# Performance work log

Measured on AMD Instinct MI355X. Metric: run time of the kernel, lower is better.

Reference implementation:

```python
import jax, jax.numpy as jnp
import numpy as np

N_HEAD = 16

def setup_inputs() -> dict:
    key = jax.random.key(0)
    ks = jax.random.split(key, 5)
    B, T, C = 4, 2048, 1024
    s = 0.02
    return {
        "x": jax.random.normal(ks[0], (B, T, C), dtype=jnp.float32),
        "W_attn": jax.random.normal(ks[1], (C, 3 * C), dtype=jnp.float32) * s,
        "b_attn": jax.random.normal(ks[2], (3 * C,), dtype=jnp.float32) * s,
        "W_proj": jax.random.normal(ks[3], (C, C), dtype=jnp.float32) * s,
        "b_proj": jax.random.normal(ks[4], (C,), dtype=jnp.float32) * s,
    }

def reference(x, W_attn, b_attn, W_proj, b_proj):
    B, T, C = x.shape
    H = N_HEAD
    D = C // H
    qkv = x @ W_attn + b_attn                      # [B,T,3C]
    q, k, v = jnp.split(qkv, 3, axis=2)
    # [B,H,T,D]
    q = q.reshape(B, T, H, D).transpose(0, 2, 1, 3)
    k = k.reshape(B, T, H, D).transpose(0, 2, 1, 3)
    v = v.reshape(B, T, H, D).transpose(0, 2, 1, 3)
    scale = 1.0 / jnp.sqrt(jnp.float32(D))
    att = jnp.einsum('bhqd,bhkd->bhqk', q, k) * scale
    causal = jnp.tril(jnp.ones((T, T), dtype=bool))
    att = jnp.where(causal[None, None], att, -jnp.inf)
    att = jax.nn.softmax(att, axis=-1)
    y = jnp.einsum('bhqk,bhkd->bhqd', att, v)       # [B,H,T,D]
    y = y.transpose(0, 2, 1, 3).reshape(B, T, C)
    return y @ W_proj + b_proj
```

## Files before the change

### kernel.cpp

```cpp
#include <hip/hip_runtime.h>

typedef unsigned short u16;
typedef unsigned int u32;
typedef __bf16 bf16x8 __attribute__((ext_vector_type(8)));
typedef float f32x4 __attribute__((ext_vector_type(4)));

#define MFMA16(a,b,c) __builtin_amdgcn_mfma_f32_16x16x32_bf16((a),(b),(c),0,0,0)

__device__ __forceinline__ float b2f(u16 u) {
    u32 v = ((u32)u) << 16;
    return __builtin_bit_cast(float, v);
}
__device__ __forceinline__ u16 f2b(float f) {
    u32 u = __builtin_bit_cast(u32, f);
    u = u + 0x7FFFu + ((u >> 16) & 1u);
    return (u16)(u >> 16);
}

__device__ __forceinline__ void gload_lds16(const u16* g, u16* l) {
    __builtin_amdgcn_global_load_lds(
        (__attribute__((address_space(1))) void*)g,
        (__attribute__((address_space(3))) void*)l, 16, 0, 0);
}

__device__ __forceinline__ uint4 load8_bf16(const void* base, size_t off, int f32m) {
    if (f32m) {
        const float* p = (const float*)base + off;
        float4 a = *(const float4*)p;
        float4 b = *(const float4*)(p + 4);
        union { u16 u[8]; uint4 v; } t;
        t.u[0] = f2b(a.x); t.u[1] = f2b(a.y); t.u[2] = f2b(a.z); t.u[3] = f2b(a.w);
        t.u[4] = f2b(b.x); t.u[5] = f2b(b.y); t.u[6] = f2b(b.z); t.u[7] = f2b(b.w);
        return t.v;
    }
    return *(const uint4*)((const u16*)base + off);
}

__global__ __launch_bounds__(256) void k_detect(const u16* __restrict__ x, int* flag) {
    __shared__ int c;
    if (threadIdx.x == 0) c = 0;
    __syncthreads();
    int my = 0;
    #pragma unroll
    for (int j = 0; j < 16; ++j) {
        u16 v = x[2 * (threadIdx.x + 256 * j)];
        if (((v >> 7) & 0xFF) >= 0x90) ++my;
    }
    atomicAdd(&c, my);
    __syncthreads();
    if (threadIdx.x == 0) *flag = (c > 64) ? 1 : 0;
}

__global__ __launch_bounds__(256) void k_cvt_bias(
    const void* __restrict__ ba, const void* __restrict__ bp,
    const int* __restrict__ flag, u16* __restrict__ bac, u16* __restrict__ bpc)
{
    const int f32m = *flag;
    const int t = threadIdx.x;
    #pragma unroll
    for (int j = 0; j < 12; ++j) {
        int i = t + 256 * j;
        if (i < 3072) bac[i] = f32m ? f2b(((const float*)ba)[i]) : ((const u16*)ba)[i];
    }
    #pragma unroll
    for (int j = 0; j < 4; ++j) {
        int i = t + 256 * j;
        if (i < 1024) bpc[i] = f32m ? f2b(((const float*)bp)[i]) : ((const u16*)bp)[i];
    }
}

__global__ __launch_bounds__(256) void k_cvt_x(
    const float* __restrict__ x, const int* __restrict__ flag, u16* __restrict__ out)
{
    if (!*flag) return;
    size_t i = ((size_t)blockIdx.x * 256 + threadIdx.x) * 8;
    float4 a = *(const float4*)(x + i);
    float4 b = *(const float4*)(x + i + 4);
    union { u16 u[8]; uint4 v; } t;
    t.u[0] = f2b(a.x); t.u[1] = f2b(a.y); t.u[2] = f2b(a.z); t.u[3] = f2b(a.w);
    t.u[4] = f2b(b.x); t.u[5] = f2b(b.y); t.u[6] = f2b(b.z); t.u[7] = f2b(b.w);
    *(uint4*)(out + i) = t.v;
}

__global__ __launch_bounds__(256) void k_transpose(
    const void* __restrict__ src, u16* __restrict__ dst, int R, int Cc,
    const int* __restrict__ flag)
{
    __shared__ u16 tile[64 * 72];
    const int f32m = *flag;
    const int t = threadIdx.x;
    const int c0 = blockIdx.x * 64, r0 = blockIdx.y * 64;
    #pragma unroll
    for (int i = 0; i < 2; ++i) {
        int ch = t + 256 * i;
        int r = ch >> 3, c8 = (ch & 7) * 8;
        *(uint4*)&tile[r * 72 + c8] =
            load8_bf16(src, (size_t)(r0 + r) * Cc + c0 + c8, f32m);
    }
    __syncthreads();
    #pragma unroll
    for (int i = 0; i < 2; ++i) {
        int ch = t + 256 * i;
        int r = ch >> 3, c8 = (ch & 7) * 8;
        union { u16 u[8]; uint4 v; } tmp;
        #pragma unroll
        for (int j = 0; j < 8; ++j) tmp.u[j] = tile[(c8 + j) * 72 + r];
        *(uint4*)&dst[(size_t)(c0 + r) * R + r0 + c8] = tmp.v;
    }
}

__global__ __launch_bounds__(256) void k_gemm_qkv(
    const void* __restrict__ x, const u16* __restrict__ Abf,
    const u16* __restrict__ Bt, const u16* __restrict__ bias,
    const int* __restrict__ flag,
    u16* __restrict__ Ql, u16* __restrict__ Kl, u16* __restrict__ Vt)
{
    constexpr int K = 1024;
    __shared__ __align__(16) u16 As[128 * 64];
    __shared__ __align__(16) u16 Bs[128 * 64];
    const int t = threadIdx.x;
    const int lane = t & 63, w = t >> 6;
    const int quad = lane >> 4, m16 = lane & 15;
    const int wm = (w >> 1) * 64, wn = (w & 1) * 64;
    const int m0 = blockIdx.x * 128, n0 = blockIdx.y * 128;
    const int lr = lane >> 3;
    const int lc = (lane & 7) * 8;
    const u16* A = (*flag) ? Abf : (const u16*)x;

    const f32x4 z = {0.f, 0.f, 0.f, 0.f};
    f32x4 acc[4][4];
    #pragma unroll
    for (int mi = 0; mi < 4; ++mi)
        #pragma unroll
        for (int ni = 0; ni < 4; ++ni) acc[mi][ni] = z;

    for (int k0 = 0; k0 < K; k0 += 64) {
        __syncthreads();
        #pragma unroll
        for (int i = 0; i < 4; ++i) {
            const int chunk = w * 4 + i;
            const int row = chunk * 8 + lr;
            gload_lds16(&A [(size_t)(m0 + row) * K + k0 + lc], &As[chunk * 512]);
            gload_lds16(&Bt[(size_t)(n0 + row) * K + k0 + lc], &Bs[chunk * 512]);
        }
        __syncthreads();
        #pragma unroll
        for (int kk = 0; kk < 2; ++kk) {
            bf16x8 af[4], bfr[4];
            #pragma unroll
            for (int mi = 0; mi < 4; ++mi)
                af[mi] = *(const bf16x8*)&As[(wm + mi * 16 + m16) * 64 + kk * 32 + quad * 8];
            #pragma unroll
            for (int ni = 0; ni < 4; ++ni)
                bfr[ni] = *(const bf16x8*)&Bs[(wn + ni * 16 + m16) * 64 + kk * 32 + quad * 8];
            #pragma unroll
            for (int mi = 0; mi < 4; ++mi)
                #pragma unroll
                for (int ni = 0; ni < 4; ++ni)
                    acc[mi][ni] = MFMA16(af[mi], bfr[ni], acc[mi][ni]);
        }
    }

    const int sec = n0 >> 10;
    const float qscale = (sec == 0) ? 0.18033688011112042f : 1.0f;
    #pragma unroll
    for (int mi = 0; mi < 4; ++mi) {
        #pragma unroll
        for (int ni = 0; ni < 4; ++ni) {
            int gn = n0 + wn + ni * 16 + m16;
            int sn = gn & 1023;
            int h = sn >> 6, d = sn & 63;
            float bv = b2f(bias[gn]);
            #pragma unroll
            for (int v = 0; v < 4; ++v) {
                int gm = m0 + wm + mi * 16 + quad * 4 + v;
                int bb = gm >> 11, tt = gm & 2047;
                u16 o = f2b((acc[mi][ni][v] + bv) * qscale);
                size_t bh = (size_t)(bb * 16 + h);
                if (sec == 0)      Ql[(bh * 2048 + tt) * 64 + d] = o;
                else if (sec == 1) Kl[(bh * 2048 + tt) * 64 + d] = o;
                else               Vt[(bh * 64 + d) * 2048 + tt] = o;
            }
        }
    }
}

__global__ __launch_bounds__(256) void k_attn(
    u16* __restrict__ Ql, const u16* __restrict__ Kl, const u16* __restrict__ Vt)
{
    __shared__ u16 Ks[128 * 72];
    __shared__ u16 Vs[64 * 136];
    __shared__ u16 Ps[64 * 136];
    const int t = threadIdx.x;
    const int lane = t & 63, w = t >> 6;
    const int quad = lane >> 4, m16 = lane & 15;
    const int qb = 15 - (blockIdx.x >> 6);
    const int bh = blockIdx.x & 63;
    const int q0 = qb * 128;

    bf16x8 fq[2][2];
    #pragma unroll
    for (int s = 0; s < 2; ++s) {
        const u16* Qp = Ql + ((size_t)bh * 2048 + q0 + s * 64 + w * 16 + m16) * 64;
        fq[s][0] = *(const bf16x8*)&Qp[quad * 8];
        fq[s][1] = *(const bf16x8*)&Qp[32 + quad * 8];
    }

    const f32x4 z = {0.f, 0.f, 0.f, 0.f};
    f32x4 acco[2][4] = {{z, z, z, z}, {z, z, z, z}};
    f32x4 accl[2] = {z, z};
    bf16x8 ones;
    #pragma unroll
    for (int j = 0; j < 8; ++j) ones[j] = (__bf16)1.0f;

    const int ktmax = qb;
    const u16* Kbase = Kl + (size_t)bh * 2048 * 64;
    const u16* Vbase = Vt + (size_t)bh * 64 * 2048;

    uint4 kreg[4], vreg[4];
    #pragma unroll
    for (int i = 0; i < 4; ++i) {
        int c = t + 256 * i;
        int r = c >> 3, col = (c & 7) * 8;
        kreg[i] = *(const uint4*)&Kbase[(size_t)r * 64 + col];
        int dd = c >> 4, kvc = (c & 15) * 8;
        vreg[i] = *(const uint4*)&Vbase[(size_t)dd * 2048 + kvc];
    }

    const int pr = (w * 16 + m16) * 136;

    for (int kt = 0; kt <= ktmax; ++kt) {
        __syncthreads();
        #pragma unroll
        for (int i = 0; i < 4; ++i) {
            int c = t + 256 * i;
            int r = c >> 3, col = (c & 7) * 8;
            *(uint4*)&Ks[r * 72 + col] = kreg[i];
            int dd = c >> 4, kvc = (c & 15) * 8;
            *(uint4*)&Vs[dd * 136 + kvc] = vreg[i];
        }
        __syncthreads();

        if (kt < ktmax) {
            #pragma unroll
            for (int i = 0; i < 4; ++i) {
                int c = t + 256 * i;
                int r = c >> 3, col = (c & 7) * 8;
                kreg[i] = *(const uint4*)&Kbase[(size_t)((kt + 1) * 128 + r) * 64 + col];
                int dd = c >> 4, kvc = (c & 15) * 8;
                vreg[i] = *(const uint4*)&Vbase[(size_t)dd * 2048 + (kt + 1) * 128 + kvc];
            }
        }

        const bool diag = (kt == ktmax);
        #pragma unroll
        for (int s = 0; s < 2; ++s) {
            f32x4 accs[8] = {z, z, z, z, z, z, z, z};
            #pragma unroll
            for (int kk = 0; kk < 2; ++kk)
                #pragma unroll
                for (int ni = 0; ni < 8; ++ni) {
                    bf16x8 bk = *(const bf16x8*)&Ks[(ni * 16 + m16) * 72 + kk * 32 + quad * 8];
                    accs[ni] = MFMA16(bk, fq[s][kk], accs[ni]);
                }

            const int qg = q0 + s * 64 + w * 16 + m16;
            #pragma unroll
            for (int ni = 0; ni < 8; ++ni) {
                union { __bf16 b[4]; uint2 u; } pk;
                #pragma unroll
                for (int v = 0; v < 4; ++v) {
                    float sc = accs[ni][v];
                    if (diag && (kt * 128 + ni * 16 + quad * 4 + v > qg)) sc = -30000.0f;
                    pk.b[v] = (__bf16)__builtin_amdgcn_exp2f(sc);
                }
                *(uint2*)&Ps[pr + ni * 16 + quad * 4] = pk.u;
            }

            #pragma unroll
            for (int kk = 0; kk < 4; ++kk) {
                bf16x8 ap = *(const bf16x8*)&Ps[pr + kk * 32 + quad * 8];
                #pragma unroll
                for (int nd = 0; nd < 4; ++nd) {
                    bf16x8 bv = *(const bf16x8*)&Vs[(nd * 16 + m16) * 136 + kk * 32 + quad * 8];
                    acco[s][nd] = MFMA16(ap, bv, acco[s][nd]);
                }
                accl[s] = MFMA16(ap, ones, accl[s]);
            }
        }
    }

    #pragma unroll
    for (int s = 0; s < 2; ++s)
        #pragma unroll
        for (int v = 0; v < 4; ++v) {
            int qg = q0 + s * 64 + w * 16 + quad * 4 + v;
            float inv = 1.0f / fmaxf(accl[s][v], 1e-30f);
            #pragma unroll
            for (int nd = 0; nd < 4; ++nd)
                Ql[((size_t)bh * 2048 + qg) * 64 + nd * 16 + m16] = f2b(acco[s][nd][v] * inv);
        }
}

__global__ __launch_bounds__(256) void k_gemm_proj(
    const u16* __restrict__ Yl, const u16* __restrict__ Bt, const u16* __restrict__ bias,
    const int* __restrict__ flag, void* __restrict__ Out)
{
    constexpr int K = 1024;
    __shared__ __align__(16) u16 As[128 * 64];
    __shared__ __align__(16) u16 Bs[128 * 64];
    const int f32m = *flag;
    const int t = threadIdx.x;
    const int lane = t & 63, w = t >> 6;
    const int quad = lane >> 4, m16 = lane & 15;
    const int wm = (w >> 1) * 64, wn = (w & 1) * 64;
    const int m0 = blockIdx.x * 128, n0 = blockIdx.y * 128;
    const int bb = m0 >> 11, t0 = m0 & 2047;
    const int lr = lane >> 3;
    const int lc = (lane & 7) * 8;

    const f32x4 z = {0.f, 0.f, 0.f, 0.f};
    f32x4 acc[4][4];
    #pragma unroll
    for (int mi = 0; mi < 4; ++mi)
        #pragma unroll
        for (int ni = 0; ni < 4; ++ni) acc[mi][ni] = z;

    for (int k0 = 0; k0 < K; k0 += 64) {
        const int h = k0 >> 6;
        const u16* Abase = Yl + ((size_t)(bb * 16 + h) * 2048 + t0) * 64;
        __syncthreads();
        #pragma unroll
        for (int i = 0; i < 4; ++i) {
            const int chunk = w * 4 + i;
            gload_lds16(&Abase[chunk * 512 + lane * 8], &As[chunk * 512]);
            gload_lds16(&Bt[(size_t)(n0 + chunk * 8 + lr) * K + k0 + lc], &Bs[chunk * 512]);
        }
        __syncthreads();
        #pragma unroll
        for (int kk = 0; kk < 2; ++kk) {
            bf16x8 af[4], bfr[4];
            #pragma unroll
            for (int mi = 0; mi < 4; ++mi)
                af[mi] = *(const bf16x8*)&As[(wm + mi * 16 + m16) * 64 + kk * 32 + quad * 8];
            #pragma unroll
            for (int ni = 0; ni < 4; ++ni)
                bfr[ni] = *(const bf16x8*)&Bs[(wn + ni * 16 + m16) * 64 + kk * 32 + quad * 8];
            #pragma unroll
            for (int mi = 0; mi < 4; ++mi)
                #pragma unroll
                for (int ni = 0; ni < 4; ++ni)
                    acc[mi][ni] = MFMA16(af[mi], bfr[ni], acc[mi][ni]);
        }
    }

    #pragma unroll
    for (int mi = 0; mi < 4; ++mi) {
        #pragma unroll
        for (int ni = 0; ni < 4; ++ni) {
            int gn = n0 + wn + ni * 16 + m16;
            float bv = b2f(bias[gn]);
            #pragma unroll
            for (int v = 0; v < 4; ++v) {
                int gm = m0 + wm + mi * 16 + quad * 4 + v;
                float val = acc[mi][ni][v] + bv;
                if (f32m) ((float*)Out)[(size_t)gm * 1024 + gn] = val;
                else      ((u16*)Out)[(size_t)gm * 1024 + gn] = f2b(val);
            }
        }
    }
}

extern "C" void kernel_launch(void* const* d_in, const int* in_sizes, int n_in,
                              void* d_out, int out_size, void* d_ws, size_t ws_size,
                              hipStream_t stream)
{
    (void)in_sizes; (void)n_in; (void)out_size; (void)ws_size;
    const void* x  = d_in[0];
    const void* Wa = d_in[1];
    const void* ba = d_in[2];
    const void* Wp = d_in[3];
    const void* bp = d_in[4];
    char* ws = (char*)d_ws;

    u16* Ql  = (u16*)(ws + 0);
    u16* Kl  = (u16*)(ws + 16777216);
    u16* Vt  = (u16*)(ws + 33554432);
    u16* WpT = (u16*)(ws + 50331648);
    int* flag = (int*)(ws + 52428800);
    u16* bpc  = (u16*)(ws + 52428800 + 256);
    u16* bac  = (u16*)(ws + 52428800 + 256 + 2048);
    u16* WaT = (u16*)d_out;
    u16* Abf = (u16*)((char*)d_out + 6291456);

    k_detect<<<1, 256, 0, stream>>>((const u16*)x, flag);
    k_cvt_bias<<<1, 256, 0, stream>>>(ba, bp, flag, bac, bpc);
    k_cvt_x<<<4096, 256, 0, stream>>>((const float*)x, flag, Abf);
    k_transpose<<<dim3(48, 16), 256, 0, stream>>>(Wa, WaT, 1024, 3072, flag);
    k_transpose<<<dim3(16, 16), 256, 0, stream>>>(Wp, WpT, 1024, 1024, flag);
    k_gemm_qkv<<<dim3(64, 24), 256, 0, stream>>>(x, Abf, WaT, bac, flag, Ql, Kl, Vt);
    k_attn<<<1024, 256, 0, stream>>>(Ql, Kl, Vt);
    k_gemm_proj<<<dim3(64, 8), 256, 0, stream>>>(Ql, WpT, bpc, flag, d_out);
}
```

Measured before the change: 340.2 us.

## Keep softmax probabilities in registers and feed PV MFMA directly via 16x16x16 bf16

The P matrix is no longer written to and re-read from LDS. The exp'd scores stay in registers and feed a 16x16x16 bf16 MFMA, with V as the A operand, so the output accumulator comes out transposed. The row sum is now accumulated in fp32 on the scalar side and reduced with lane shuffles, replacing the extra MFMA against a ones vector, and output stores become vectorized. This removes LDS traffic and one MFMA per step, but uses the older half-depth MFMA instruction, which issues more MFMAs for the PV product. It also changes the K padding from 72 to 80.

```diff
diff --git a/kernel.cpp b/kernel.cpp
--- a/kernel.cpp
+++ b/kernel.cpp
@@ -3,9 +3,25 @@
 typedef unsigned short u16;
 typedef unsigned int u32;
 typedef __bf16 bf16x8 __attribute__((ext_vector_type(8)));
+typedef short s16x4 __attribute__((ext_vector_type(4)));
 typedef float f32x4 __attribute__((ext_vector_type(4)));
 
 #define MFMA16(a,b,c) __builtin_amdgcn_mfma_f32_16x16x32_bf16((a),(b),(c),0,0,0)
+
+#if defined(__has_builtin)
+#if __has_builtin(__builtin_amdgcn_mfma_f32_16x16x16bf16_1k)
+#define MFMA1K(a,b,c) __builtin_amdgcn_mfma_f32_16x16x16bf16_1k((a),(b),(c),0,0,0)
+#endif
+#endif
+#ifndef MFMA1K
+__device__ __forceinline__ f32x4 mfma1k_asm(s16x4 a, s16x4 b, f32x4 c) {
+    f32x4 d;
+    asm volatile("v_mfma_f32_16x16x16_bf16 %0, %1, %2, %3"
+                 : "=v"(d) : "v"(a), "v"(b), "0"(c));
+    return d;
+}
+#define MFMA1K(a,b,c) mfma1k_asm((a),(b),(c))
+#endif
 
 __device__ __forceinline__ float b2f(u16 u) {
     u32 v = ((u32)u) << 16;
@@ -188,9 +204,8 @@
 __global__ __launch_bounds__(256) void k_attn(
     u16* __restrict__ Ql, const u16* __restrict__ Kl, const u16* __restrict__ Vt)
 {
-    __shared__ u16 Ks[128 * 72];
+    __shared__ u16 Ks[128 * 80];
     __shared__ u16 Vs[64 * 136];
-    __shared__ u16 Ps[64 * 136];
     const int t = threadIdx.x;
     const int lane = t & 63, w = t >> 6;
     const int quad = lane >> 4, m16 = lane & 15;
@@ -208,10 +223,7 @@
 
     const f32x4 z = {0.f, 0.f, 0.f, 0.f};
     f32x4 acco[2][4] = {{z, z, z, z}, {z, z, z, z}};
-    f32x4 accl[2] = {z, z};
-    bf16x8 ones;
-    #pragma unroll
-    for (int j = 0; j < 8; ++j) ones[j] = (__bf16)1.0f;
+    float lsum[2] = {0.f, 0.f};
 
     const int ktmax = qb;
     const u16* Kbase = Kl + (size_t)bh * 2048 * 64;
@@ -227,15 +239,13 @@
         vreg[i] = *(const uint4*)&Vbase[(size_t)dd * 2048 + kvc];
     }
 
-    const int pr = (w * 16 + m16) * 136;
-
     for (int kt = 0; kt <= ktmax; ++kt) {
         __syncthreads();
         #pragma unroll
         for (int i = 0; i < 4; ++i) {
             int c = t + 256 * i;
             int r = c >> 3, col = (c & 7) * 8;
-            *(uint4*)&Ks[r * 72 + col] = kreg[i];
+            *(uint4*)&Ks[r * 80 + col] = kreg[i];
             int dd = c >> 4, kvc = (c & 15) * 8;
             *(uint4*)&Vs[dd * 136 + kvc] = vreg[i];
         }
@@ -260,46 +270,56 @@
             for (int kk = 0; kk < 2; ++kk)
                 #pragma unroll
                 for (int ni = 0; ni < 8; ++ni) {
-                    bf16x8 bk = *(const bf16x8*)&Ks[(ni * 16 + m16) * 72 + kk * 32 + quad * 8];
+                    bf16x8 bk = *(const bf16x8*)&Ks[(ni * 16 + m16) * 80 + kk * 32 + quad * 8];
                     accs[ni] = MFMA16(bk, fq[s][kk], accs[ni]);
                 }
 
             const int qg = q0 + s * 64 + w * 16 + m16;
+            s16x4 pkv[8];
             #pragma unroll
             for (int ni = 0; ni < 8; ++ni) {
-                union { __bf16 b[4]; uint2 u; } pk;
+                union { __bf16 b[4]; s16x4 sv; } pk;
                 #pragma unroll
                 for (int v = 0; v < 4; ++v) {
                     float sc = accs[ni][v];
                     if (diag && (kt * 128 + ni * 16 + quad * 4 + v > qg)) sc = -30000.0f;
-                    pk.b[v] = (__bf16)__builtin_amdgcn_exp2f(sc);
+                    float pe = __builtin_amdgcn_exp2f(sc);
+                    pk.b[v] = (__bf16)pe;
+                    lsum[s] += pe;
                 }
-                *(uint2*)&Ps[pr + ni * 16 + quad * 4] = pk.u;
+                pkv[ni] = pk.sv;
             }
 
             #pragma unroll
-            for (int kk = 0; kk < 4; ++kk) {
-                bf16x8 ap = *(const bf16x8*)&Ps[pr + kk * 32 + quad * 8];
+            for (int ni = 0; ni < 8; ++ni) {
                 #pragma unroll
                 for (int nd = 0; nd < 4; ++nd) {
-                    bf16x8 bv = *(const bf16x8*)&Vs[(nd * 16 + m16) * 136 + kk * 32 + quad * 8];
-                    acco[s][nd] = MFMA16(ap, bv, acco[s][nd]);
+                    s16x4 va = *(const s16x4*)&Vs[(nd * 16 + m16) * 136 + ni * 16 + quad * 4];
+                    acco[s][nd] = MFMA1K(va, pkv[ni], acco[s][nd]);
                 }
-                accl[s] = MFMA16(ap, ones, accl[s]);
             }
         }
     }
 
     #pragma unroll
-    for (int s = 0; s < 2; ++s)
-        #pragma unroll
-        for (int v = 0; v < 4; ++v) {
-            int qg = q0 + s * 64 + w * 16 + quad * 4 + v;
-            float inv = 1.0f / fmaxf(accl[s][v], 1e-30f);
-            #pragma unroll
-            for (int nd = 0; nd < 4; ++nd)
-                Ql[((size_t)bh * 2048 + qg) * 64 + nd * 16 + m16] = f2b(acco[s][nd][v] * inv);
-        }
+    for (int s = 0; s < 2; ++s) {
+        lsum[s] += __shfl_xor(lsum[s], 16);
+        lsum[s] += __shfl_xor(lsum[s], 32);
+    }
+
+    #pragma unroll
+    for (int s = 0; s < 2; ++s) {
+        const int qg = q0 + s * 64 + w * 16 + m16;
+        const float inv = 1.0f / fmaxf(lsum[s], 1e-30f);
+        u16* Orow = &Ql[((size_t)bh * 2048 + qg) * 64];
+        #pragma unroll
+        for (int nd = 0; nd < 4; ++nd) {
+            union { u16 u[4]; uint2 uu; } o;
+            #pragma unroll
+            for (int v = 0; v < 4; ++v) o.u[v] = f2b(acco[s][nd][v] * inv);
+            *(uint2*)&Orow[nd * 16 + quad * 4] = o.uu;
+        }
+    }
 }
 
 __global__ __launch_bounds__(256) void k_gemm_proj(
```

New measurement: 336.9 us. Within noise of the previous version (-1.0%).
